# Optimization experiments

Measured on AMD Instinct MI355X. Metric: run time of the kernel, lower is better.

Reference implementation:

```python
import jax, jax.numpy as jnp
import numpy as np

K = 2            # top-k experts
TEMPERATURE = 1.0
EPS = 1e-9


def setup_inputs() -> dict:
    key = jax.random.key(0)
    k1, k2 = jax.random.split(key)
    B, S, D = 4, 4096, 4096
    G, E = 4, 64
    x = jax.random.normal(k1, (B, S, D), dtype=jnp.float32)
    # stacked gate weights, one [E, D] Linear weight per gate head
    W = jax.random.normal(k2, (G, E, D), dtype=jnp.float32) * 0.02
    return {"x": x, "W": W}


def reference(x, W):
    # per-head logits over experts: [B, S, G, E]; jitter disabled (eval / jitter_noise=0)
    logits = jnp.einsum('bsd,ged->bsge', x, W) * (1.0 / TEMPERATURE)
    probs = jax.nn.softmax(logits, axis=-1)          # softmax per head
    probs_full = probs.mean(axis=2)                  # consensus over heads: [B, S, E]
    topk_vals, idx = jax.lax.top_k(probs_full, K)    # sorted descending, matches aten.topk
    den = jnp.sum(topk_vals, axis=-1, keepdims=True)
    scores = topk_vals / jnp.maximum(den, EPS)       # clamp_min(den, 1e-9)
    pf = jax.lax.stop_gradient(probs_full)           # aux stats under no_grad
    importance = pf.mean(axis=(0, 1))                # [E]
    load = (pf > 0.0).astype(pf.dtype).mean(axis=(0, 1))  # [E]
    return idx, scores, probs_full, importance, load
```

## Files before the change

kernel.cpp:

```cpp
#include <hip/hip_runtime.h>

typedef _Float16 f16x8 __attribute__((ext_vector_type(8)));
typedef float    f32x4 __attribute__((ext_vector_type(4)));

#define MROWS 16384
#define NCOLS 256
#define KDIM  4096
#define BM    128
#define BK    32
#define LDA   40

#define OUT_SCORES 32768
#define OUT_PF     65536
#define OUT_IMP    1114112
#define OUT_LOAD   1114176

__global__ __launch_bounds__(256) void wprep(const float* __restrict__ W,
                                             _Float16* __restrict__ wfHi,
                                             _Float16* __restrict__ wfLo) {
    int t  = blockIdx.x * 256 + threadIdx.x;
    int n  = t >> 9;
    int k8 = t & 511;
    const float* src = W + ((size_t)n * KDIM + (size_t)k8 * 8);
    f16x8 hi, lo;
#pragma unroll
    for (int j = 0; j < 8; ++j) {
        float x = src[j];
        _Float16 h = (_Float16)x;
        hi[j] = h;
        lo[j] = (_Float16)(x - (float)h);
    }
    int NT  = n >> 4;
    int ksg = k8 >> 2;
    int l   = (n & 15) + ((k8 & 3) << 4);
    size_t dst = ((size_t)(ksg * 16 + NT) * 64 + (size_t)l) * 8;
    *(f16x8*)(wfHi + dst) = hi;
    *(f16x8*)(wfLo + dst) = lo;
}

__global__ __launch_bounds__(256, 2) void gemm3(const float* __restrict__ X,
        const _Float16* __restrict__ wfHi, const _Float16* __restrict__ wfLo,
        float* __restrict__ lsplit, int kQ) {
    __shared__ _Float16 aHi[BM * LDA];
    __shared__ _Float16 aLo[BM * LDA];

    const int tid  = threadIdx.x;
    const int lane = tid & 63;
    const int w    = tid >> 6;
    const int mt   = blockIdx.x & 127;
    const int s    = blockIdx.x >> 7;
    const int m0   = mt * BM;
    const int k0   = s * kQ;
    const int iters = kQ / BK;

    f32x4 acc[8][4];
#pragma unroll
    for (int a = 0; a < 8; ++a)
#pragma unroll
        for (int b = 0; b < 4; ++b) acc[a][b] = (f32x4){0.f, 0.f, 0.f, 0.f};

    const int sr = tid >> 1;
    const int sh = tid & 1;
    const float* xrow = X + ((size_t)(m0 + sr) * KDIM + (size_t)k0 + sh * 16);
    _Float16* wAH = aHi + sr * LDA + sh * 16;
    _Float16* wAL = aLo + sr * LDA + sh * 16;

    const _Float16* rAH = aHi + (lane & 15) * LDA + (lane >> 4) * 8;
    const _Float16* rAL = aLo + (lane & 15) * LDA + (lane >> 4) * 8;

    size_t bbase = (((size_t)(k0 >> 5) * 16 + (size_t)w * 4) * 64 + (size_t)lane) * 8;
    const _Float16* pBH = wfHi + bbase;
    const _Float16* pBL = wfLo + bbase;

    for (int i = 0; i < iters; ++i) {
        f16x8 bH[4], bL[4];
#pragma unroll
        for (int ni = 0; ni < 4; ++ni) {
            bH[ni] = *(const f16x8*)(pBH + (size_t)ni * 512);
            bL[ni] = *(const f16x8*)(pBL + (size_t)ni * 512);
        }
        pBH += 16 * 512;
        pBL += 16 * 512;

        float xv[16];
        const float* xp = xrow + (size_t)i * BK;
#pragma unroll
        for (int q = 0; q < 4; ++q) {
            f32x4 v = *(const f32x4*)(xp + q * 4);
            xv[q*4+0] = v[0]; xv[q*4+1] = v[1]; xv[q*4+2] = v[2]; xv[q*4+3] = v[3];
        }
        f16x8 h0, h1, l0, l1;
#pragma unroll
        for (int j = 0; j < 8; ++j) {
            _Float16 ha = (_Float16)xv[j];
            h0[j] = ha; l0[j] = (_Float16)(xv[j] - (float)ha);
            _Float16 hb = (_Float16)xv[8 + j];
            h1[j] = hb; l1[j] = (_Float16)(xv[8 + j] - (float)hb);
        }
        __syncthreads();
        *(f16x8*)(wAH)     = h0;
        *(f16x8*)(wAH + 8) = h1;
        *(f16x8*)(wAL)     = l0;
        *(f16x8*)(wAL + 8) = l1;
        __syncthreads();

#pragma unroll
        for (int mi = 0; mi < 8; ++mi) {
            f16x8 aH = *(const f16x8*)(rAH + mi * 16 * LDA);
            f16x8 aL = *(const f16x8*)(rAL + mi * 16 * LDA);
#pragma unroll
            for (int ni = 0; ni < 4; ++ni) {
                acc[mi][ni] = __builtin_amdgcn_mfma_f32_16x16x32_f16(aH, bH[ni], acc[mi][ni], 0, 0, 0);
                acc[mi][ni] = __builtin_amdgcn_mfma_f32_16x16x32_f16(aH, bL[ni], acc[mi][ni], 0, 0, 0);
                acc[mi][ni] = __builtin_amdgcn_mfma_f32_16x16x32_f16(aL, bH[ni], acc[mi][ni], 0, 0, 0);
            }
        }
    }

    float* outp = lsplit + (size_t)s * ((size_t)MROWS * NCOLS);
#pragma unroll
    for (int mi = 0; mi < 8; ++mi) {
#pragma unroll
        for (int ni = 0; ni < 4; ++ni) {
            int col   = w * 64 + ni * 16 + (lane & 15);
            int rbase = m0 + mi * 16 + ((lane >> 4) << 2);
#pragma unroll
            for (int r = 0; r < 4; ++r)
                outp[(size_t)(rbase + r) * NCOLS + col] = acc[mi][ni][r];
        }
    }
}

__global__ __launch_bounds__(256) void finalize(const float* __restrict__ lsplit,
                                                int nsplit, float* __restrict__ out) {
    __shared__ float sImp[64], sLoad[64];
    const int tid = threadIdx.x;
    if (tid < 64) { sImp[tid] = 0.f; sLoad[tid] = 0.f; }
    __syncthreads();

    const int i   = tid & 15;
    const int grp = tid >> 4;
    const int r   = blockIdx.x * 16 + grp;

    float v[16];
#pragma unroll
    for (int t = 0; t < 16; ++t) {
        size_t off = (size_t)r * 256 + (size_t)i + 16 * t;
        float a = lsplit[off];
        for (int s = 1; s < nsplit; ++s)
            a += lsplit[(size_t)s * ((size_t)MROWS * NCOLS) + off];
        v[t] = a;
    }

    float hm[4];
#pragma unroll
    for (int g = 0; g < 4; ++g) {
        float m = fmaxf(fmaxf(v[4*g], v[4*g+1]), fmaxf(v[4*g+2], v[4*g+3]));
#pragma unroll
        for (int msk = 1; msk < 16; msk <<= 1)
            m = fmaxf(m, __shfl_xor(m, msk));
        hm[g] = m;
    }
    float p[16], inv[4];
#pragma unroll
    for (int g = 0; g < 4; ++g) {
        float sa = 0.f;
#pragma unroll
        for (int q = 0; q < 4; ++q) { p[4*g+q] = __expf(v[4*g+q] - hm[g]); sa += p[4*g+q]; }
#pragma unroll
        for (int msk = 1; msk < 16; msk <<= 1)
            sa += __shfl_xor(sa, msk);
        inv[g] = 1.f / sa;
    }

    float pf[4];
#pragma unroll
    for (int et = 0; et < 4; ++et) {
        pf[et] = 0.25f * (p[et] * inv[0] + p[4+et] * inv[1] + p[8+et] * inv[2] + p[12+et] * inv[3]);
        out[OUT_PF + (size_t)r * 64 + i + 16 * et] = pf[et];
        atomicAdd(&sImp[i + 16 * et], pf[et]);
        atomicAdd(&sLoad[i + 16 * et], pf[et] > 0.f ? 1.f : 0.f);
    }

    float v1 = -3.4e38f, v2 = -3.4e38f; int e1 = 0, e2 = 0;
#pragma unroll
    for (int et = 0; et < 4; ++et) {
        int e = i + 16 * et; float val = pf[et];
        if (val > v1) { v2 = v1; e2 = e1; v1 = val; e1 = e; }
        else if (val > v2) { v2 = val; e2 = e; }
    }
#pragma unroll
    for (int msk = 1; msk < 16; msk <<= 1) {
        float o1 = __shfl_xor(v1, msk); int oe1 = __shfl_xor(e1, msk);
        float o2 = __shfl_xor(v2, msk); int oe2 = __shfl_xor(e2, msk);
        bool ob = (o1 > v1) || (o1 == v1 && oe1 < e1);
        if (ob) {
            bool vb = (v1 > o2) || (v1 == o2 && e1 < oe2);
            v2 = vb ? v1 : o2; e2 = vb ? e1 : oe2;
            v1 = o1; e1 = oe1;
        } else {
            bool nb = (o1 > v2) || (o1 == v2 && oe1 < e2);
            v2 = nb ? o1 : v2; e2 = nb ? oe1 : e2;
        }
    }
    if (i == 0) {
        float den = fmaxf(v1 + v2, 1e-9f);
        out[(size_t)r * 2]              = (float)e1;
        out[(size_t)r * 2 + 1]          = (float)e2;
        out[OUT_SCORES + (size_t)r * 2]     = v1 / den;
        out[OUT_SCORES + (size_t)r * 2 + 1] = v2 / den;
    }
    __syncthreads();
    if (tid < 64) {
        atomicAdd(out + OUT_IMP  + tid, sImp[tid]  * (1.0f / 16384.0f));
        atomicAdd(out + OUT_LOAD + tid, sLoad[tid] * (1.0f / 16384.0f));
    }
}

extern "C" void kernel_launch(void* const* d_in, const int* in_sizes, int n_in,
                              void* d_out, int out_size, void* d_ws, size_t ws_size,
                              hipStream_t stream) {
    const float* X = (const float*)d_in[0];
    const float* W = (const float*)d_in[1];
    float* out = (float*)d_out;
    char* ws = (char*)d_ws;

    _Float16* wfHi = (_Float16*)ws;
    _Float16* wfLo = (_Float16*)(ws + (2u << 20));
    float* lsplit  = (float*)(ws + (4u << 20));

    const size_t per = 16u << 20;
    int nsplit = (ws_size >= (4u << 20) + 4 * per) ? 4
               : (ws_size >= (4u << 20) + 2 * per) ? 2 : 1;

    hipMemsetAsync((void*)(out + OUT_IMP), 0, 128 * sizeof(float), stream);

    wprep<<<512, 256, 0, stream>>>(W, wfHi, wfLo);
    gemm3<<<128 * nsplit, 256, 0, stream>>>(X, wfHi, wfLo, lsplit, KDIM / nsplit);
    finalize<<<1024, 256, 0, stream>>>(lsplit, nsplit, out);
}
```

Before: 455.5 us.

## Double-buffer A tile in LDS and prefetch next X slice during MFMA

Result: no change. 463.3 us (+1.7%).

```diff
diff --git a/kernel.cpp b/kernel.cpp
--- a/kernel.cpp
+++ b/kernel.cpp
@@ -18,10 +18,13 @@
 __global__ __launch_bounds__(256) void wprep(const float* __restrict__ W,
                                              _Float16* __restrict__ wfHi,
                                              _Float16* __restrict__ wfLo) {
-    int t  = blockIdx.x * 256 + threadIdx.x;
-    int n  = t >> 9;
-    int k8 = t & 511;
-    const float* src = W + ((size_t)n * KDIM + (size_t)k8 * 8);
+    int t   = blockIdx.x * 256 + threadIdx.x;
+    int l   = t & 63;
+    int NT  = (t >> 6) & 15;
+    int ksg = t >> 10;
+    int n   = NT * 16 + (l & 15);
+    int k   = ksg * 32 + ((l >> 4) << 3);
+    const float* src = W + ((size_t)n * KDIM + (size_t)k);
     f16x8 hi, lo;
 #pragma unroll
     for (int j = 0; j < 8; ++j) {
@@ -30,19 +33,15 @@
         hi[j] = h;
         lo[j] = (_Float16)(x - (float)h);
     }
-    int NT  = n >> 4;
-    int ksg = k8 >> 2;
-    int l   = (n & 15) + ((k8 & 3) << 4);
-    size_t dst = ((size_t)(ksg * 16 + NT) * 64 + (size_t)l) * 8;
-    *(f16x8*)(wfHi + dst) = hi;
-    *(f16x8*)(wfLo + dst) = lo;
+    *(f16x8*)(wfHi + (size_t)t * 8) = hi;
+    *(f16x8*)(wfLo + (size_t)t * 8) = lo;
 }
 
 __global__ __launch_bounds__(256, 2) void gemm3(const float* __restrict__ X,
         const _Float16* __restrict__ wfHi, const _Float16* __restrict__ wfLo,
         float* __restrict__ lsplit, int kQ) {
-    __shared__ _Float16 aHi[BM * LDA];
-    __shared__ _Float16 aLo[BM * LDA];
+    __shared__ _Float16 aHi[2][BM * LDA];
+    __shared__ _Float16 aLo[2][BM * LDA];
 
     const int tid  = threadIdx.x;
     const int lane = tid & 63;
@@ -62,17 +61,46 @@
     const int sr = tid >> 1;
     const int sh = tid & 1;
     const float* xrow = X + ((size_t)(m0 + sr) * KDIM + (size_t)k0 + sh * 16);
-    _Float16* wAH = aHi + sr * LDA + sh * 16;
-    _Float16* wAL = aLo + sr * LDA + sh * 16;
-
-    const _Float16* rAH = aHi + (lane & 15) * LDA + (lane >> 4) * 8;
-    const _Float16* rAL = aLo + (lane & 15) * LDA + (lane >> 4) * 8;
+    const int woff = sr * LDA + sh * 16;
+
+    const int roff = (lane & 15) * LDA + (lane >> 4) * 8;
 
     size_t bbase = (((size_t)(k0 >> 5) * 16 + (size_t)w * 4) * 64 + (size_t)lane) * 8;
     const _Float16* pBH = wfHi + bbase;
     const _Float16* pBL = wfLo + bbase;
 
+    {
+        f32x4 v[4];
+#pragma unroll
+        for (int q = 0; q < 4; ++q) v[q] = *(const f32x4*)(xrow + q * 4);
+        f16x8 h0, h1, l0, l1;
+#pragma unroll
+        for (int j = 0; j < 8; ++j) {
+            float a = v[j >> 2][j & 3];
+            _Float16 ha = (_Float16)a;
+            h0[j] = ha; l0[j] = (_Float16)(a - (float)ha);
+            float b = v[2 + (j >> 2)][j & 3];
+            _Float16 hb = (_Float16)b;
+            h1[j] = hb; l1[j] = (_Float16)(b - (float)hb);
+        }
+        *(f16x8*)(&aHi[0][woff])     = h0;
+        *(f16x8*)(&aHi[0][woff + 8]) = h1;
+        *(f16x8*)(&aLo[0][woff])     = l0;
+        *(f16x8*)(&aLo[0][woff + 8]) = l1;
+    }
+    __syncthreads();
+
     for (int i = 0; i < iters; ++i) {
+        const int cur = i & 1;
+
+        f32x4 nx[4];
+        const bool more = (i + 1 < iters);
+        if (more) {
+            const float* xp = xrow + (size_t)(i + 1) * BK;
+#pragma unroll
+            for (int q = 0; q < 4; ++q) nx[q] = *(const f32x4*)(xp + q * 4);
+        }
+
         f16x8 bH[4], bL[4];
 #pragma unroll
         for (int ni = 0; ni < 4; ++ni) {
@@ -82,32 +110,10 @@
         pBH += 16 * 512;
         pBL += 16 * 512;
 
-        float xv[16];
-        const float* xp = xrow + (size_t)i * BK;
-#pragma unroll
-        for (int q = 0; q < 4; ++q) {
-            f32x4 v = *(const f32x4*)(xp + q * 4);
-            xv[q*4+0] = v[0]; xv[q*4+1] = v[1]; xv[q*4+2] = v[2]; xv[q*4+3] = v[3];
-        }
-        f16x8 h0, h1, l0, l1;
-#pragma unroll
-        for (int j = 0; j < 8; ++j) {
-            _Float16 ha = (_Float16)xv[j];
-            h0[j] = ha; l0[j] = (_Float16)(xv[j] - (float)ha);
-            _Float16 hb = (_Float16)xv[8 + j];
-            h1[j] = hb; l1[j] = (_Float16)(xv[8 + j] - (float)hb);
-        }
-        __syncthreads();
-        *(f16x8*)(wAH)     = h0;
-        *(f16x8*)(wAH + 8) = h1;
-        *(f16x8*)(wAL)     = l0;
-        *(f16x8*)(wAL + 8) = l1;
-        __syncthreads();
-
 #pragma unroll
         for (int mi = 0; mi < 8; ++mi) {
-            f16x8 aH = *(const f16x8*)(rAH + mi * 16 * LDA);
-            f16x8 aL = *(const f16x8*)(rAL + mi * 16 * LDA);
+            f16x8 aH = *(const f16x8*)(&aHi[cur][roff + mi * 16 * LDA]);
+            f16x8 aL = *(const f16x8*)(&aLo[cur][roff + mi * 16 * LDA]);
 #pragma unroll
             for (int ni = 0; ni < 4; ++ni) {
                 acc[mi][ni] = __builtin_amdgcn_mfma_f32_16x16x32_f16(aH, bH[ni], acc[mi][ni], 0, 0, 0);
@@ -115,6 +121,25 @@
                 acc[mi][ni] = __builtin_amdgcn_mfma_f32_16x16x32_f16(aL, bH[ni], acc[mi][ni], 0, 0, 0);
             }
         }
+
+        if (more) {
+            const int nxt = cur ^ 1;
+            f16x8 h0, h1, l0, l1;
+#pragma unroll
+            for (int j = 0; j < 8; ++j) {
+                float a = nx[j >> 2][j & 3];
+                _Float16 ha = (_Float16)a;
+                h0[j] = ha; l0[j] = (_Float16)(a - (float)ha);
+                float b = nx[2 + (j >> 2)][j & 3];
+                _Float16 hb = (_Float16)b;
+                h1[j] = hb; l1[j] = (_Float16)(b - (float)hb);
+            }
+            *(f16x8*)(&aHi[nxt][woff])     = h0;
+            *(f16x8*)(&aHi[nxt][woff + 8]) = h1;
+            *(f16x8*)(&aLo[nxt][woff])     = l0;
+            *(f16x8*)(&aLo[nxt][woff + 8]) = l1;
+        }
+        __syncthreads();
     }
 
     float* outp = lsplit + (size_t)s * ((size_t)MROWS * NCOLS);
```
